# Optimization experiments

Hardware: AMD Instinct MI355X
Metric: run time of the kernel (lower is better)

The kernel has to match this reference:

```python
import jax, jax.numpy as jnp
import numpy as np

B, N, C_IN, C_INTER = 32, 2048, 512, 512


def setup_inputs() -> dict:
    key = jax.random.key(0)
    ks = jax.random.split(key, 10)
    s_in = 1.0 / np.sqrt(C_IN)
    s_int = 1.0 / np.sqrt(C_INTER)
    return {
        "query": jax.random.normal(ks[0], (B, N, C_IN), jnp.float32),
        "key": jax.random.normal(ks[1], (B, N, C_IN), jnp.float32),
        "Wq": jax.random.normal(ks[2], (C_IN, C_INTER), jnp.float32) * s_in,
        "bq": jnp.zeros((C_INTER,), jnp.float32),
        "Wk": jax.random.normal(ks[3], (C_IN, C_INTER), jnp.float32) * s_in,
        "bk": jnp.zeros((C_INTER,), jnp.float32),
        "Wv": jax.random.normal(ks[4], (C_IN, C_INTER), jnp.float32) * s_in,
        "bv": jnp.zeros((C_INTER,), jnp.float32),
        "Wo": jax.random.normal(ks[5], (C_INTER, C_INTER), jnp.float32) * s_int,
        "bo": jnp.zeros((C_INTER,), jnp.float32),
    }


def reference(query, key, Wq, bq, Wk, bk, Wv, bv, Wo, bo):
    value = key  # value defaults to key in original forward
    q = jnp.einsum("bnc,cd->bnd", query, Wq) + bq   # [B,N,D]
    k = jnp.einsum("bnc,cd->bnd", key, Wk) + bk
    v = jnp.einsum("bnc,cd->bnd", value, Wv) + bv
    d = q.shape[-1]
    # non-standard scaling: divide by d (not sqrt(d))
    scores = jnp.einsum("bqd,bkd->bqk", q, k) / d    # [B,N,N]
    attn = jax.nn.softmax(scores, axis=-1)
    n_kv = attn.shape[-1]
    # second non-standard scaling: divide by number of keys
    out = jnp.einsum("bqk,bkd->bqd", attn, v) / n_kv
    return jnp.einsum("bnd,de->bne", out, Wo) + bo
```

## Files before the change

kernel.cpp:

```cpp
#include <hip/hip_runtime.h>
#include <stdint.h>

typedef unsigned short u16;
typedef __attribute__((ext_vector_type(8))) short bf16x8;
typedef __attribute__((ext_vector_type(4))) float f32x4;

__device__ __forceinline__ float bf2f(u16 u) {
  union { unsigned int i; float f; } v; v.i = ((unsigned int)u) << 16; return v.f;
}
__device__ __forceinline__ u16 f2bf(float f) {
  union { float f; unsigned int i; } v; v.f = f;
  unsigned int x = v.i;
  return (u16)((x + 0x7fffu + ((x >> 16) & 1u)) >> 16);
}

__device__ __forceinline__ void async16(const void* g, void* l) {
  __builtin_amdgcn_global_load_lds(
      (const __attribute__((address_space(1))) void*)g,
      (__attribute__((address_space(3))) void*)l, 16, 0, 0);
}

__global__ __launch_bounds__(256) void cast_f32_to_bf16(
    const float* __restrict__ x, u16* __restrict__ y, long n) {
  long i = ((long)blockIdx.x * blockDim.x + threadIdx.x) * 8;
  long stride = (long)gridDim.x * blockDim.x * 8;
  for (long j = i; j < n; j += stride) {
    float4 a = ((const float4*)(x + j))[0];
    float4 b = ((const float4*)(x + j))[1];
    unsigned int p0 = (unsigned)f2bf(a.x) | ((unsigned)f2bf(a.y) << 16);
    unsigned int p1 = (unsigned)f2bf(a.z) | ((unsigned)f2bf(a.w) << 16);
    unsigned int p2 = (unsigned)f2bf(b.x) | ((unsigned)f2bf(b.y) << 16);
    unsigned int p3 = (unsigned)f2bf(b.z) | ((unsigned)f2bf(b.w) << 16);
    *(uint4*)(y + j) = make_uint4(p0, p1, p2, p3);
  }
}

__global__ __launch_bounds__(256) void castKT(
    const float* __restrict__ Kin, u16* __restrict__ Kb, u16* __restrict__ KbT) {
  __shared__ u16 tile[32][34];
  int t = threadIdx.x;
  long b = blockIdx.z;
  int n0 = blockIdx.x * 32, c0 = blockIdx.y * 32;
  int nr = t >> 3, c4 = (t & 7) * 4;
  float4 v = *(const float4*)(Kin + (b * 2048 + n0 + nr) * 512 + c0 + c4);
  unsigned q0 = f2bf(v.x), q1 = f2bf(v.y), q2 = f2bf(v.z), q3 = f2bf(v.w);
  *(uint2*)(Kb + (b * 2048 + n0 + nr) * 512 + c0 + c4) =
      make_uint2(q0 | (q1 << 16), q2 | (q3 << 16));
  tile[nr][c4] = (u16)q0; tile[nr][c4 + 1] = (u16)q1;
  tile[nr][c4 + 2] = (u16)q2; tile[nr][c4 + 3] = (u16)q3;
  __syncthreads();
  int cr = t >> 3, n4 = (t & 7) * 4;
  unsigned r0 = tile[n4][cr], r1 = tile[n4 + 1][cr];
  unsigned r2 = tile[n4 + 2][cr], r3 = tile[n4 + 3][cr];
  *(uint2*)(KbT + (b * 512 + c0 + cr) * 2048 + n0 + n4) =
      make_uint2(r0 | (r1 << 16), r2 | (r3 << 16));
}

__global__ __launch_bounds__(256) void smallGT(
    const float* __restrict__ Ai, const float* __restrict__ Bi, u16* __restrict__ C) {
  __shared__ float As[16][65], Bs[16][65];
  int t = threadIdx.x;
  int i0 = blockIdx.y * 16, j0 = blockIdx.x * 16;
  int r = t >> 4, c4 = (t & 15) * 4;
  int ty = t >> 4, tx = t & 15;
  float acc = 0.f;
  for (int d0 = 0; d0 < 512; d0 += 64) {
    float4 a = *(const float4*)(Ai + (i0 + r) * 512 + d0 + c4);
    float4 b = *(const float4*)(Bi + (j0 + r) * 512 + d0 + c4);
    __syncthreads();
    As[r][c4] = a.x; As[r][c4 + 1] = a.y; As[r][c4 + 2] = a.z; As[r][c4 + 3] = a.w;
    Bs[r][c4] = b.x; Bs[r][c4 + 1] = b.y; Bs[r][c4 + 2] = b.z; Bs[r][c4 + 3] = b.w;
    __syncthreads();
#pragma unroll
    for (int d = 0; d < 64; ++d) acc += As[ty][d] * Bs[tx][d];
  }
  C[(i0 + ty) * 512 + j0 + tx] = f2bf(acc);
}

__global__ __launch_bounds__(256) void smallW2T(
    const float* __restrict__ Wv, const float* __restrict__ Wo, u16* __restrict__ C) {
  __shared__ float Vs[16][65];
  __shared__ float Os[64][17];
  int t = threadIdx.x;
  int k0 = blockIdx.x * 16, n0 = blockIdx.y * 16;
  int r = t >> 4, c4 = (t & 15) * 4;
  int dd = t >> 2, nn4 = (t & 3) * 4;
  int ty = t >> 4, tx = t & 15;
  float acc = 0.f;
  for (int d0 = 0; d0 < 512; d0 += 64) {
    float4 a = *(const float4*)(Wv + (k0 + r) * 512 + d0 + c4);
    float4 b = *(const float4*)(Wo + (long)(d0 + dd) * 512 + n0 + nn4);
    __syncthreads();
    Vs[r][c4] = a.x; Vs[r][c4 + 1] = a.y; Vs[r][c4 + 2] = a.z; Vs[r][c4 + 3] = a.w;
    Os[dd][nn4] = b.x; Os[dd][nn4 + 1] = b.y; Os[dd][nn4 + 2] = b.z; Os[dd][nn4 + 3] = b.w;
    __syncthreads();
#pragma unroll
    for (int d = 0; d < 64; ++d) acc += Vs[tx][d] * Os[d][ty];
  }
  C[(n0 + ty) * 512 + k0 + tx] = f2bf(acc);
}

__global__ __launch_bounds__(256) void wveck(
    const float* __restrict__ Wk, const float* __restrict__ bq, float* __restrict__ wv) {
  int c = blockIdx.x, t = threadIdx.x;
  float s = 0.f;
  for (int d = t; d < 512; d += 256) s += Wk[c * 512 + d] * bq[d];
  for (int off = 32; off; off >>= 1) s += __shfl_xor(s, off);
  __shared__ float r4[4];
  if ((t & 63) == 0) r4[t >> 6] = s;
  __syncthreads();
  if (t == 0) wv[c] = (r4[0] + r4[1] + r4[2] + r4[3]) * (1.0f / 512.0f);
}

__global__ __launch_bounds__(256) void cveck(
    const float* __restrict__ Wo, const float* __restrict__ bv,
    const float* __restrict__ bo, float* __restrict__ c2) {
  int e = blockIdx.x * 256 + threadIdx.x;
  float s = 0.f;
  for (int d = 0; d < 512; ++d) s += bv[d] * Wo[d * 512 + e];
  c2[e] = s * (1.0f / 2048.0f) + bo[e];
}

__global__ __launch_bounds__(256) void betak(
    const u16* __restrict__ Kb, const float* __restrict__ wv, float* __restrict__ beta) {
  __shared__ float ws[512];
  int t = threadIdx.x, lane = t & 63, wid = t >> 6;
  ws[t] = wv[t];
  ws[t + 256] = wv[t + 256];
  __syncthreads();
  long row = (long)blockIdx.x * 4 + wid;
  bf16x8 v = *(const bf16x8*)(Kb + row * 512 + lane * 8);
  float s = 0.f;
#pragma unroll
  for (int j = 0; j < 8; ++j) s += bf2f((u16)v[j]) * ws[lane * 8 + j];
  for (int off = 32; off; off >>= 1) s += __shfl_xor(s, off);
  if (lane == 0) beta[row] = s;
}

template <int MODE>
__global__ __launch_bounds__(256, 3) void gemm(
    const u16* __restrict__ A, const u16* __restrict__ B,
    const float* __restrict__ bias, long sBias, void* __restrict__ Cout,
    int N, int K, long sA, long sB, long sC, float scale) {
  __shared__ __align__(16) char lds[2][24576];
  const int t = threadIdx.x;
  const int lane = t & 63;
  const int w = t >> 6;
  const int wm = w >> 1;
  const int wn = w & 1;
  const long z = blockIdx.z;
  const long m0 = (long)blockIdx.x * 256;
  const int n0 = blockIdx.y * 128;
  const int nt = K >> 5;

  const int srow = w * 16 + (lane >> 2);
  const int koff = 8 * ((lane & 3) ^ ((lane >> 3) & 3));
  const u16* pa = A + z * sA + (m0 + srow) * (long)K + koff;
  const u16* pb = B + z * sB + ((long)(n0 + srow)) * K + koff;
  const int ldsW = w * 1024;

  const int fr = lane & 15;
  const int kb = (lane >> 4) * 16;
  const int sw = ((fr >> 1) & 3) << 4;
  const int aoff = (wm * 128 + fr) * 64 + (kb ^ sw);
  const int boff = 16384 + (wn * 64 + fr) * 64 + (kb ^ sw);

  f32x4 acc[8][4] = {};

  {
    char* d = lds[0] + ldsW;
#pragma unroll
    for (int c = 0; c < 4; ++c) async16(pa + (long)c * 64 * K, d + c * 4096);
#pragma unroll
    for (int c = 0; c < 2; ++c) async16(pb + (long)c * 64 * K, d + 16384 + c * 4096);
    pa += 32; pb += 32;
  }
  __syncthreads();

  int cur = 0;
  for (int tt = 0; tt < nt; ++tt) {
    if (tt + 1 < nt) {
      char* d = lds[cur ^ 1] + ldsW;
#pragma unroll
      for (int c = 0; c < 4; ++c) async16(pa + (long)c * 64 * K, d + c * 4096);
#pragma unroll
      for (int c = 0; c < 2; ++c) async16(pb + (long)c * 64 * K, d + 16384 + c * 4096);
      pa += 32; pb += 32;
    }
    const char* rb = lds[cur];
    bf16x8 bf[4];
#pragma unroll
    for (int ni = 0; ni < 4; ++ni)
      bf[ni] = *(const bf16x8*)(rb + boff + ni * 1024);
    __builtin_amdgcn_s_setprio(1);
#pragma unroll
    for (int mi = 0; mi < 8; ++mi) {
      bf16x8 af = *(const bf16x8*)(rb + aoff + mi * 1024);
#pragma unroll
      for (int ni = 0; ni < 4; ++ni)
        acc[mi][ni] = __builtin_amdgcn_mfma_f32_16x16x32_bf16(af, bf[ni], acc[mi][ni], 0, 0, 0);
    }
    __builtin_amdgcn_s_setprio(0);
    __syncthreads();
    cur ^= 1;
  }

  const int er = (lane >> 4) * 4;
  const int ec = lane & 15;
  if (MODE == 0) {
    u16* Ep = (u16*)lds;
    u16* Cp = (u16*)Cout + z * sC;
    float bvv[4];
#pragma unroll
    for (int ni = 0; ni < 4; ++ni)
      bvv[ni] = bias ? bias[z * sBias + n0 + wn * 64 + ni * 16 + ec] : 0.0f;
#pragma unroll
    for (int p = 0; p < 2; ++p) {
      __syncthreads();
      if (wm == p) {
#pragma unroll
        for (int mi = 0; mi < 8; ++mi)
#pragma unroll
          for (int ni = 0; ni < 4; ++ni)
#pragma unroll
            for (int i = 0; i < 4; ++i)
              Ep[(mi * 16 + er + i) * 136 + wn * 64 + ni * 16 + ec] =
                  f2bf(acc[mi][ni][i] * scale + bvv[ni]);
      }
      __syncthreads();
#pragma unroll
      for (int s = 0; s < 8; ++s) {
        int idx = s * 256 + t;
        int R = idx >> 4;
        int j = idx & 15;
        uint4 d = *(const uint4*)(Ep + R * 136 + j * 8);
        *(uint4*)(Cp + (m0 + p * 128 + R) * (long)N + n0 + j * 8) = d;
      }
    }
  } else {
    float* Cp = (float*)Cout + z * sC;
#pragma unroll
    for (int mi = 0; mi < 8; ++mi)
#pragma unroll
      for (int ni = 0; ni < 4; ++ni)
#pragma unroll
        for (int i = 0; i < 4; ++i) {
          long gm = m0 + wm * 128 + mi * 16 + er + i;
          int gc = n0 + wn * 64 + ni * 16 + ec;
          float val = acc[mi][ni][i] * scale;
          if (bias) val += bias[gc];
          Cp[gm * (long)N + gc] = val;
        }
  }
}

__global__ __launch_bounds__(256) void softmax_rows(u16* __restrict__ S, float inv) {
  long row = blockIdx.x;
  u16* p = S + row * 2048;
  int t = threadIdx.x;
  int lane = t & 63, wv = t >> 6;

  uint4 raw = ((const uint4*)p)[t];
  unsigned int wd[4] = {raw.x, raw.y, raw.z, raw.w};
  float v[8];
#pragma unroll
  for (int j = 0; j < 4; ++j) {
    v[2 * j]     = bf2f((u16)(wd[j] & 0xffffu));
    v[2 * j + 1] = bf2f((u16)(wd[j] >> 16));
  }
  float mx = v[0];
#pragma unroll
  for (int j = 1; j < 8; ++j) mx = fmaxf(mx, v[j]);
  for (int off = 32; off; off >>= 1) mx = fmaxf(mx, __shfl_xor(mx, off));
  __shared__ float rmax[4], rsum[4];
  if (lane == 0) rmax[wv] = mx;
  __syncthreads();
  mx = fmaxf(fmaxf(rmax[0], rmax[1]), fmaxf(rmax[2], rmax[3]));

  float e[8], s = 0.f;
#pragma unroll
  for (int j = 0; j < 8; ++j) { e[j] = __expf(v[j] - mx); s += e[j]; }
  for (int off = 32; off; off >>= 1) s += __shfl_xor(s, off);
  if (lane == 0) rsum[wv] = s;
  __syncthreads();
  s = rsum[0] + rsum[1] + rsum[2] + rsum[3];

  float r = inv / s;
  unsigned int o[4];
#pragma unroll
  for (int j = 0; j < 4; ++j)
    o[j] = (unsigned)f2bf(e[2 * j] * r) | ((unsigned)f2bf(e[2 * j + 1] * r) << 16);
  ((uint4*)p)[t] = make_uint4(o[0], o[1], o[2], o[3]);
}

extern "C" void kernel_launch(void* const* d_in, const int* in_sizes, int n_in,
                              void* d_out, int out_size, void* d_ws, size_t ws_size,
                              hipStream_t stream) {
  const float* query = (const float*)d_in[0];
  const float* key_  = (const float*)d_in[1];
  const float* Wq = (const float*)d_in[2];
  const float* bq = (const float*)d_in[3];
  const float* Wk = (const float*)d_in[4];
  const float* bk = (const float*)d_in[5];
  const float* Wv = (const float*)d_in[6];
  const float* bv = (const float*)d_in[7];
  const float* Wo = (const float*)d_in[8];
  const float* bo = (const float*)d_in[9];
  (void)bk;
  float* out = (float*)d_out;

  const long tokE = 65536L * 512;
  const long bstride = 2048L * 512;

  char* ws = (char*)d_ws;
  u16* Qb   = (u16*)(ws);
  u16* Kb   = (u16*)(ws + 67108864L);
  u16* KbT  = (u16*)(ws + 134217728L);
  u16* GT   = (u16*)(ws + 201326592L);
  u16* W2T  = (u16*)(ws + 201850880L);
  float* wv   = (float*)(ws + 202375168L);
  float* c2   = (float*)(ws + 202377216L);
  float* beta = (float*)(ws + 202379264L);
  char* Sbase = ws + 203423744L;
  u16* attn = Qb;

  u16* qb = (u16*)d_out;

  long s_avail = (long)ws_size - 203423744L;
  int g = (int)(s_avail / 8388608L);
  if (g < 1) g = 1;
  if (g > 32) g = 32;

  cast_f32_to_bf16<<<16384, 256, 0, stream>>>(query, Qb, tokE);
  castKT<<<dim3(64, 16, 32), 256, 0, stream>>>(key_, Kb, KbT);
  smallGT<<<dim3(32, 32), 256, 0, stream>>>(Wk, Wq, GT);
  smallW2T<<<dim3(32, 32), 256, 0, stream>>>(Wv, Wo, W2T);
  wveck<<<512, 256, 0, stream>>>(Wk, bq, wv);
  cveck<<<2, 256, 0, stream>>>(Wo, bv, bo, c2);
  betak<<<16384, 256, 0, stream>>>(Kb, wv, beta);

  gemm<0><<<dim3(256, 4, 1), 256, 0, stream>>>(Qb, GT, nullptr, 0, qb,
                                               512, 512, 0, 0, 0, 1.0f);

  for (int b0 = 0; b0 < 32; b0 += g) {
    int bc = (32 - b0 < g) ? (32 - b0) : g;
    u16* Sg = (u16*)Sbase;
    gemm<0><<<dim3(8, 16, bc), 256, 0, stream>>>(
        qb + (long)b0 * bstride, Kb + (long)b0 * bstride,
        beta + (long)b0 * 2048, 2048, Sg, 2048, 512,
        bstride, bstride, 2048L * 2048, 1.0f / 512.0f);
    softmax_rows<<<bc * 2048, 256, 0, stream>>>(Sg, 1.0f / 2048.0f);
    gemm<0><<<dim3(8, 4, bc), 256, 0, stream>>>(
        Sg, KbT + (long)b0 * bstride, nullptr, 0,
        attn + (long)b0 * bstride, 512, 2048,
        2048L * 2048, bstride, bstride, 1.0f);
  }

  gemm<2><<<dim3(256, 4, 1), 256, 0, stream>>>(attn, W2T, c2, 0, out,
                                               512, 512, 0, 0, 0, 1.0f);
}
```

Baseline: 769.2 us.

## Add XCD-aware tile remapping, nontemporal stores, LDS-staged fp32 epilogue, wave-per-row softmax

Flattens the GEMM grid and remaps workgroups so each batch is pinned to one XCD (when the batch count is a multiple of 8), with a selectable N-fast tile order for the PV GEMM. This is meant to improve L2 reuse of K/V and Q tiles. It also switches output stores to nontemporal, stages the fp32 output epilogue through LDS for coalesced 16-byte stores, and rewrites softmax so one wave handles a whole row without block barriers. Nontemporal stores can hurt when a later kernel immediately rereads the data, such as S feeding softmax and the PV GEMM.

```diff
diff --git a/kernel.cpp b/kernel.cpp
--- a/kernel.cpp
+++ b/kernel.cpp
@@ -4,6 +4,8 @@
 typedef unsigned short u16;
 typedef __attribute__((ext_vector_type(8))) short bf16x8;
 typedef __attribute__((ext_vector_type(4))) float f32x4;
+typedef __attribute__((ext_vector_type(2))) unsigned int u32x2;
+typedef __attribute__((ext_vector_type(4))) unsigned int u32x4;
 
 __device__ __forceinline__ float bf2f(u16 u) {
   union { unsigned int i; float f; } v; v.i = ((unsigned int)u) << 16; return v.f;
@@ -27,11 +29,12 @@
   for (long j = i; j < n; j += stride) {
     float4 a = ((const float4*)(x + j))[0];
     float4 b = ((const float4*)(x + j))[1];
-    unsigned int p0 = (unsigned)f2bf(a.x) | ((unsigned)f2bf(a.y) << 16);
-    unsigned int p1 = (unsigned)f2bf(a.z) | ((unsigned)f2bf(a.w) << 16);
-    unsigned int p2 = (unsigned)f2bf(b.x) | ((unsigned)f2bf(b.y) << 16);
-    unsigned int p3 = (unsigned)f2bf(b.z) | ((unsigned)f2bf(b.w) << 16);
-    *(uint4*)(y + j) = make_uint4(p0, p1, p2, p3);
+    u32x4 o;
+    o.x = (unsigned)f2bf(a.x) | ((unsigned)f2bf(a.y) << 16);
+    o.y = (unsigned)f2bf(a.z) | ((unsigned)f2bf(a.w) << 16);
+    o.z = (unsigned)f2bf(b.x) | ((unsigned)f2bf(b.y) << 16);
+    o.w = (unsigned)f2bf(b.z) | ((unsigned)f2bf(b.w) << 16);
+    __builtin_nontemporal_store(o, (u32x4*)(y + j));
   }
 }
 
@@ -44,16 +47,16 @@
   int nr = t >> 3, c4 = (t & 7) * 4;
   float4 v = *(const float4*)(Kin + (b * 2048 + n0 + nr) * 512 + c0 + c4);
   unsigned q0 = f2bf(v.x), q1 = f2bf(v.y), q2 = f2bf(v.z), q3 = f2bf(v.w);
-  *(uint2*)(Kb + (b * 2048 + n0 + nr) * 512 + c0 + c4) =
-      make_uint2(q0 | (q1 << 16), q2 | (q3 << 16));
+  u32x2 o1; o1.x = q0 | (q1 << 16); o1.y = q2 | (q3 << 16);
+  __builtin_nontemporal_store(o1, (u32x2*)(Kb + (b * 2048 + n0 + nr) * 512 + c0 + c4));
   tile[nr][c4] = (u16)q0; tile[nr][c4 + 1] = (u16)q1;
   tile[nr][c4 + 2] = (u16)q2; tile[nr][c4 + 3] = (u16)q3;
   __syncthreads();
   int cr = t >> 3, n4 = (t & 7) * 4;
   unsigned r0 = tile[n4][cr], r1 = tile[n4 + 1][cr];
   unsigned r2 = tile[n4 + 2][cr], r3 = tile[n4 + 3][cr];
-  *(uint2*)(KbT + (b * 512 + c0 + cr) * 2048 + n0 + n4) =
-      make_uint2(r0 | (r1 << 16), r2 | (r3 << 16));
+  u32x2 o2; o2.x = r0 | (r1 << 16); o2.y = r2 | (r3 << 16);
+  __builtin_nontemporal_store(o2, (u32x2*)(KbT + (b * 512 + c0 + cr) * 2048 + n0 + n4));
 }
 
 __global__ __launch_bounds__(256) void smallGT(
@@ -141,16 +144,32 @@
 __global__ __launch_bounds__(256, 3) void gemm(
     const u16* __restrict__ A, const u16* __restrict__ B,
     const float* __restrict__ bias, long sBias, void* __restrict__ Cout,
-    int N, int K, long sA, long sB, long sC, float scale) {
+    int N, int K, long sA, long sB, long sC, float scale,
+    int mT, int nT, int Z, int nfast) {
   __shared__ __align__(16) char lds[2][24576];
   const int t = threadIdx.x;
   const int lane = t & 63;
   const int w = t >> 6;
   const int wm = w >> 1;
   const int wn = w & 1;
-  const long z = blockIdx.z;
-  const long m0 = (long)blockIdx.x * 256;
-  const int n0 = blockIdx.y * 128;
+
+  const int wg = blockIdx.x;
+  const int nb = mT * nT;
+  long z; int within;
+  if (Z > 1 && (Z & 7) == 0) {
+    int xcd = wg & 7;
+    int sub = wg >> 3;
+    z = (long)(sub / nb) * 8 + xcd;
+    within = sub % nb;
+  } else {
+    z = wg / nb;
+    within = wg % nb;
+  }
+  int bx, by;
+  if (nfast) { by = within % nT; bx = within / nT; }
+  else       { bx = within % mT; by = within / mT; }
+  const long m0 = (long)bx * 256;
+  const int n0 = by * 128;
   const int nt = K >> 5;
 
   const int srow = w * 16 + (lane >> 2);
@@ -207,13 +226,13 @@
 
   const int er = (lane >> 4) * 4;
   const int ec = lane & 15;
+  float bvv[4];
+#pragma unroll
+  for (int ni = 0; ni < 4; ++ni)
+    bvv[ni] = bias ? bias[z * sBias + n0 + wn * 64 + ni * 16 + ec] : 0.0f;
   if (MODE == 0) {
     u16* Ep = (u16*)lds;
     u16* Cp = (u16*)Cout + z * sC;
-    float bvv[4];
-#pragma unroll
-    for (int ni = 0; ni < 4; ++ni)
-      bvv[ni] = bias ? bias[z * sBias + n0 + wn * 64 + ni * 16 + ec] : 0.0f;
 #pragma unroll
     for (int p = 0; p < 2; ++p) {
       __syncthreads();
@@ -233,64 +252,79 @@
         int idx = s * 256 + t;
         int R = idx >> 4;
         int j = idx & 15;
-        uint4 d = *(const uint4*)(Ep + R * 136 + j * 8);
-        *(uint4*)(Cp + (m0 + p * 128 + R) * (long)N + n0 + j * 8) = d;
+        u32x4 d = *(const u32x4*)(Ep + R * 136 + j * 8);
+        __builtin_nontemporal_store(
+            d, (u32x4*)(Cp + (m0 + p * 128 + R) * (long)N + n0 + j * 8));
       }
     }
   } else {
+    float* Ep = (float*)lds;
     float* Cp = (float*)Cout + z * sC;
 #pragma unroll
-    for (int mi = 0; mi < 8; ++mi)
-#pragma unroll
-      for (int ni = 0; ni < 4; ++ni)
-#pragma unroll
-        for (int i = 0; i < 4; ++i) {
-          long gm = m0 + wm * 128 + mi * 16 + er + i;
-          int gc = n0 + wn * 64 + ni * 16 + ec;
-          float val = acc[mi][ni][i] * scale;
-          if (bias) val += bias[gc];
-          Cp[gm * (long)N + gc] = val;
+    for (int p = 0; p < 4; ++p) {
+      __syncthreads();
+      if (wm == (p >> 1)) {
+#pragma unroll
+        for (int mi2 = 0; mi2 < 4; ++mi2) {
+          int mi = (p & 1) * 4 + mi2;
+#pragma unroll
+          for (int ni = 0; ni < 4; ++ni)
+#pragma unroll
+            for (int i = 0; i < 4; ++i)
+              Ep[(mi2 * 16 + er + i) * 132 + wn * 64 + ni * 16 + ec] =
+                  acc[mi][ni][i] * scale + bvv[ni];
         }
+      }
+      __syncthreads();
+#pragma unroll
+      for (int s = 0; s < 8; ++s) {
+        int idx = s * 256 + t;
+        int R = idx >> 5;
+        int j = idx & 31;
+        f32x4 d = *(const f32x4*)(Ep + R * 132 + j * 4);
+        __builtin_nontemporal_store(
+            d, (f32x4*)(Cp + (m0 + p * 64 + R) * (long)N + n0 + j * 4));
+      }
+    }
   }
 }
 
 __global__ __launch_bounds__(256) void softmax_rows(u16* __restrict__ S, float inv) {
-  long row = blockIdx.x;
-  u16* p = S + row * 2048;
   int t = threadIdx.x;
   int lane = t & 63, wv = t >> 6;
-
-  uint4 raw = ((const uint4*)p)[t];
-  unsigned int wd[4] = {raw.x, raw.y, raw.z, raw.w};
-  float v[8];
-#pragma unroll
-  for (int j = 0; j < 4; ++j) {
-    v[2 * j]     = bf2f((u16)(wd[j] & 0xffffu));
-    v[2 * j + 1] = bf2f((u16)(wd[j] >> 16));
+  long row = (long)blockIdx.x * 4 + wv;
+  u16* p = S + row * 2048;
+  uint4 raw[4];
+#pragma unroll
+  for (int q = 0; q < 4; ++q) raw[q] = ((const uint4*)p)[lane + 64 * q];
+  float v[32];
+#pragma unroll
+  for (int q = 0; q < 4; ++q) {
+    unsigned wd[4] = {raw[q].x, raw[q].y, raw[q].z, raw[q].w};
+#pragma unroll
+    for (int j = 0; j < 4; ++j) {
+      v[q * 8 + 2 * j]     = bf2f((u16)(wd[j] & 0xffffu));
+      v[q * 8 + 2 * j + 1] = bf2f((u16)(wd[j] >> 16));
+    }
   }
   float mx = v[0];
 #pragma unroll
-  for (int j = 1; j < 8; ++j) mx = fmaxf(mx, v[j]);
+  for (int j = 1; j < 32; ++j) mx = fmaxf(mx, v[j]);
   for (int off = 32; off; off >>= 1) mx = fmaxf(mx, __shfl_xor(mx, off));
-  __shared__ float rmax[4], rsum[4];
-  if (lane == 0) rmax[wv] = mx;
-  __syncthreads();
-  mx = fmaxf(fmaxf(rmax[0], rmax[1]), fmaxf(rmax[2], rmax[3]));
-
-  float e[8], s = 0.f;
-#pragma unroll
-  for (int j = 0; j < 8; ++j) { e[j] = __expf(v[j] - mx); s += e[j]; }
+  float s = 0.f;
+#pragma unroll
+  for (int j = 0; j < 32; ++j) { v[j] = __expf(v[j] - mx); s += v[j]; }
   for (int off = 32; off; off >>= 1) s += __shfl_xor(s, off);
-  if (lane == 0) rsum[wv] = s;
-  __syncthreads();
-  s = rsum[0] + rsum[1] + rsum[2] + rsum[3];
-
   float r = inv / s;
-  unsigned int o[4];
-#pragma unroll
-  for (int j = 0; j < 4; ++j)
-    o[j] = (unsigned)f2bf(e[2 * j] * r) | ((unsigned)f2bf(e[2 * j + 1] * r) << 16);
-  ((uint4*)p)[t] = make_uint4(o[0], o[1], o[2], o[3]);
+#pragma unroll
+  for (int q = 0; q < 4; ++q) {
+    unsigned o[4];
+#pragma unroll
+    for (int j = 0; j < 4; ++j)
+      o[j] = (unsigned)f2bf(v[q * 8 + 2 * j] * r) |
+             ((unsigned)f2bf(v[q * 8 + 2 * j + 1] * r) << 16);
+    ((uint4*)p)[lane + 64 * q] = make_uint4(o[0], o[1], o[2], o[3]);
+  }
 }
 
 extern "C" void kernel_launch(void* const* d_in, const int* in_sizes, int n_in,
@@ -330,6 +364,7 @@
   int g = (int)(s_avail / 8388608L);
   if (g < 1) g = 1;
   if (g > 32) g = 32;
+  if (g >= 8) g &= ~7;
 
   cast_f32_to_bf16<<<16384, 256, 0, stream>>>(query, Qb, tokE);
   castKT<<<dim3(64, 16, 32), 256, 0, stream>>>(key_, Kb, KbT);
@@ -339,23 +374,23 @@
   cveck<<<2, 256, 0, stream>>>(Wo, bv, bo, c2);
   betak<<<16384, 256, 0, stream>>>(Kb, wv, beta);
 
-  gemm<0><<<dim3(256, 4, 1), 256, 0, stream>>>(Qb, GT, nullptr, 0, qb,
-                                               512, 512, 0, 0, 0, 1.0f);
+  gemm<0><<<256 * 4, 256, 0, stream>>>(Qb, GT, nullptr, 0, qb,
+                                       512, 512, 0, 0, 0, 1.0f, 256, 4, 1, 0);
 
   for (int b0 = 0; b0 < 32; b0 += g) {
     int bc = (32 - b0 < g) ? (32 - b0) : g;
     u16* Sg = (u16*)Sbase;
-    gemm<0><<<dim3(8, 16, bc), 256, 0, stream>>>(
+    gemm<0><<<8 * 16 * bc, 256, 0, stream>>>(
         qb + (long)b0 * bstride, Kb + (long)b0 * bstride,
         beta + (long)b0 * 2048, 2048, Sg, 2048, 512,
-        bstride, bstride, 2048L * 2048, 1.0f / 512.0f);
-    softmax_rows<<<bc * 2048, 256, 0, stream>>>(Sg, 1.0f / 2048.0f);
-    gemm<0><<<dim3(8, 4, bc), 256, 0, stream>>>(
+        bstride, bstride, 2048L * 2048, 1.0f / 512.0f, 8, 16, bc, 0);
+    softmax_rows<<<bc * 512, 256, 0, stream>>>(Sg, 1.0f / 2048.0f);
+    gemm<0><<<8 * 4 * bc, 256, 0, stream>>>(
         Sg, KbT + (long)b0 * bstride, nullptr, 0,
         attn + (long)b0 * bstride, 512, 2048,
-        2048L * 2048, bstride, bstride, 1.0f);
-  }
-
-  gemm<2><<<dim3(256, 4, 1), 256, 0, stream>>>(attn, W2T, c2, 0, out,
-                                               512, 512, 0, 0, 0, 1.0f);
-}
+        2048L * 2048, bstride, bstride, 1.0f, 8, 4, bc, 1);
+  }
+
+  gemm<2><<<256 * 4, 256, 0, stream>>>(attn, W2T, c2, 0, out,
+                                       512, 512, 0, 0, 0, 1.0f, 256, 4, 1, 0);
+}
```

Result: faster. 716.5 us (-6.9%).
